# Kernel tuning notes

Measured on AMD Instinct MI355X. Metric: run time of the kernel, lower is better.

## Reference

```python
import jax, jax.numpy as jnp
import numpy as np

BATCH, IN, OUT, P = 8192, 1024, 1024, 8

def setup_inputs() -> dict:
    key = jax.random.key(0)
    k1, k2, k3 = jax.random.split(key, 3)
    x = jax.random.normal(k1, (BATCH, IN), dtype=jnp.float32)
    # per-(output,input) basis coefficients, init ~ randn*0.1 as in torch module
    coefficients = jax.random.normal(k2, (OUT, IN, P), dtype=jnp.float32) * 0.1
    weights = jax.random.normal(k3, (OUT, IN), dtype=jnp.float32)
    return {"x": x, "coefficients": coefficients, "weights": weights}

def reference(x, coefficients, weights):
    # out[b,o] = sum_i x[b,i] * (sum_p coef[o,i,p]) * weights[o,i]
    # == x @ (coef_sum * weights)^T  -- single fused GEMM
    w_eff = coefficients.sum(axis=-1) * weights  # [O, I]
    return jnp.einsum('bi,oi->bo', x, w_eff)
```

## Files before the change

kernel.cpp:

```cpp
#include <hip/hip_runtime.h>
#include <hip/hip_bf16.h>
#include <stdint.h>

#define BATCH 8192
#define IN    1024
#define OUTD  1024
#define PBASIS 8

typedef __attribute__((ext_vector_type(8))) short bf16x8;
typedef __attribute__((ext_vector_type(4))) float floatx4;

__device__ __forceinline__ unsigned short f2bf(float f) {
    union { float f; unsigned u; } v; v.f = f;
    unsigned u = v.u;
    u += 0x7fffu + ((u >> 16) & 1u);
    return (unsigned short)(u >> 16);
}

__global__ void prep_kernel(const float* __restrict__ x,
                            const float* __restrict__ coef,
                            const float* __restrict__ w,
                            unsigned short* __restrict__ xb,
                            unsigned short* __restrict__ weff) {
    int b = blockIdx.x;
    int tid = threadIdx.x;
    if (b < 4096) {
        int idx = b * 256 + tid;
        const float4* p = (const float4*)(x + (size_t)idx * 8);
        float4 a = p[0], c = p[1];
        uint4 o;
        o.x = (unsigned)f2bf(a.x) | ((unsigned)f2bf(a.y) << 16);
        o.y = (unsigned)f2bf(a.z) | ((unsigned)f2bf(a.w) << 16);
        o.z = (unsigned)f2bf(c.x) | ((unsigned)f2bf(c.y) << 16);
        o.w = (unsigned)f2bf(c.z) | ((unsigned)f2bf(c.w) << 16);
        ((uint4*)xb)[idx] = o;
    } else {
        int idx = (b - 4096) * 256 + tid;
        size_t e0 = (size_t)idx * 2;
        const float4* c4 = (const float4*)(coef + e0 * PBASIS);
        float4 a = c4[0], bb = c4[1], c = c4[2], d = c4[3];
        float s0 = (a.x + a.y + a.z + a.w) + (bb.x + bb.y + bb.z + bb.w);
        float s1 = (c.x + c.y + c.z + c.w) + (d.x + d.y + d.z + d.w);
        float2 ww = ((const float2*)w)[idx];
        unsigned b0 = f2bf(s0 * ww.x);
        unsigned b1 = f2bf(s1 * ww.y);
        ((unsigned*)weff)[idx] = b0 | (b1 << 16);
    }
}

__global__ __launch_bounds__(256, 2) void gemm_bt(
        const unsigned short* __restrict__ A,
        const unsigned short* __restrict__ B,
        float* __restrict__ C) {
    constexpr int K = IN, BK = 64;
    constexpr int ES = 132;
    __shared__ __align__(16) char smem[32768];
    unsigned short* As = (unsigned short*)smem;
    unsigned short* Bs = As + 128 * BK;
    float* ebuf = (float*)smem;

    const int tid  = threadIdx.x;
    const int bm   = blockIdx.x, bn = blockIdx.y;
    const int lane = tid & 63;
    const int wave = tid >> 6;
    const int wm   = wave & 1, wn = wave >> 1;
    const int t    = lane & 15;
    const int q    = lane >> 4;
    const int r8   = t & 7;

    int G0 = tid,       r0 = G0 >> 3, c0 = G0 & 7, s0i = r0 * 8 + (c0 ^ (r0 & 7));
    int G1 = 256 + tid, r1 = G1 >> 3, c1 = G1 & 7, s1i = r1 * 8 + (c1 ^ (r1 & 7));
    int G2 = 512 + tid, r2 = G2 >> 3, c2 = G2 & 7, s2i = r2 * 8 + (c2 ^ (r2 & 7));
    int G3 = 768 + tid, r3 = G3 >> 3, c3 = G3 & 7, s3i = r3 * 8 + (c3 ^ (r3 & 7));

    const unsigned short* gA0 = A + (size_t)(bm * 128 + r0) * K + c0 * 8;
    const unsigned short* gA1 = A + (size_t)(bm * 128 + r1) * K + c1 * 8;
    const unsigned short* gA2 = A + (size_t)(bm * 128 + r2) * K + c2 * 8;
    const unsigned short* gA3 = A + (size_t)(bm * 128 + r3) * K + c3 * 8;
    const unsigned short* gB0 = B + (size_t)(bn * 128 + r0) * K + c0 * 8;
    const unsigned short* gB1 = B + (size_t)(bn * 128 + r1) * K + c1 * 8;
    const unsigned short* gB2 = B + (size_t)(bn * 128 + r2) * K + c2 * 8;
    const unsigned short* gB3 = B + (size_t)(bn * 128 + r3) * K + c3 * 8;

    unsigned short* lA0 = As + s0i * 8;  unsigned short* lB0 = Bs + s0i * 8;
    unsigned short* lA1 = As + s1i * 8;  unsigned short* lB1 = Bs + s1i * 8;
    unsigned short* lA2 = As + s2i * 8;  unsigned short* lB2 = Bs + s2i * 8;
    unsigned short* lA3 = As + s3i * 8;  unsigned short* lB3 = Bs + s3i * 8;

    const unsigned short* aB0 = As + (wm * 64 + t) * BK + ((0 + q) ^ r8) * 8;
    const unsigned short* aB1 = As + (wm * 64 + t) * BK + ((4 + q) ^ r8) * 8;
    const unsigned short* bB0 = Bs + (wn * 64 + t) * BK + ((0 + q) ^ r8) * 8;
    const unsigned short* bB1 = Bs + (wn * 64 + t) * BK + ((4 + q) ^ r8) * 8;

    floatx4 acc[4][4];
#pragma unroll
    for (int i = 0; i < 4; ++i)
#pragma unroll
        for (int j = 0; j < 4; ++j)
            acc[i][j] = (floatx4){0.f, 0.f, 0.f, 0.f};

#define COMPUTE()                                                   \
    {                                                               \
        bf16x8 af0, af1, af2, af3, ag0, ag1, ag2, ag3;              \
        bf16x8 bf0, bf1, bf2, bf3, bg0, bg1, bg2, bg3;              \
        af0 = *(const bf16x8*)(aB0 + 0 * 1024);                     \
        af1 = *(const bf16x8*)(aB0 + 1 * 1024);                     \
        af2 = *(const bf16x8*)(aB0 + 2 * 1024);                     \
        af3 = *(const bf16x8*)(aB0 + 3 * 1024);                     \
        ag0 = *(const bf16x8*)(aB1 + 0 * 1024);                     \
        ag1 = *(const bf16x8*)(aB1 + 1 * 1024);                     \
        ag2 = *(const bf16x8*)(aB1 + 2 * 1024);                     \
        ag3 = *(const bf16x8*)(aB1 + 3 * 1024);                     \
        bf0 = *(const bf16x8*)(bB0 + 0 * 1024);                     \
        bf1 = *(const bf16x8*)(bB0 + 1 * 1024);                     \
        bf2 = *(const bf16x8*)(bB0 + 2 * 1024);                     \
        bf3 = *(const bf16x8*)(bB0 + 3 * 1024);                     \
        bg0 = *(const bf16x8*)(bB1 + 0 * 1024);                     \
        bg1 = *(const bf16x8*)(bB1 + 1 * 1024);                     \
        bg2 = *(const bf16x8*)(bB1 + 2 * 1024);                     \
        bg3 = *(const bf16x8*)(bB1 + 3 * 1024);                     \
        bf16x8 afv[4] = {af0, af1, af2, af3};                       \
        bf16x8 agv[4] = {ag0, ag1, ag2, ag3};                       \
        bf16x8 bfv[4] = {bf0, bf1, bf2, bf3};                       \
        bf16x8 bgv[4] = {bg0, bg1, bg2, bg3};                       \
        _Pragma("unroll")                                           \
        for (int i = 0; i < 4; ++i)                                 \
            _Pragma("unroll")                                       \
            for (int j = 0; j < 4; ++j) {                           \
                acc[i][j] = __builtin_amdgcn_mfma_f32_16x16x32_bf16(\
                    afv[i], bfv[j], acc[i][j], 0, 0, 0);            \
                acc[i][j] = __builtin_amdgcn_mfma_f32_16x16x32_bf16(\
                    agv[i], bgv[j], acc[i][j], 0, 0, 0);            \
            }                                                       \
    }

    uint4 ca0, ca1, ca2, ca3, cb0, cb1, cb2, cb3;
    uint4 pa0, pa1, pa2, pa3, pb0, pb1, pb2, pb3;

    ca0 = *(const uint4*)gA0; ca1 = *(const uint4*)gA1;
    ca2 = *(const uint4*)gA2; ca3 = *(const uint4*)gA3;
    cb0 = *(const uint4*)gB0; cb1 = *(const uint4*)gB1;
    cb2 = *(const uint4*)gB2; cb3 = *(const uint4*)gB3;

    for (int it = 0; it < K / (2 * BK); ++it) {
        const int k1 = ((2 * it + 1) * BK);
        const int k2 = ((2 * it + 2) * BK) & (K - 1);
        *(uint4*)lA0 = ca0; *(uint4*)lA1 = ca1; *(uint4*)lA2 = ca2; *(uint4*)lA3 = ca3;
        *(uint4*)lB0 = cb0; *(uint4*)lB1 = cb1; *(uint4*)lB2 = cb2; *(uint4*)lB3 = cb3;
        __syncthreads();
        pa0 = *(const uint4*)(gA0 + k1); pa1 = *(const uint4*)(gA1 + k1);
        pa2 = *(const uint4*)(gA2 + k1); pa3 = *(const uint4*)(gA3 + k1);
        pb0 = *(const uint4*)(gB0 + k1); pb1 = *(const uint4*)(gB1 + k1);
        pb2 = *(const uint4*)(gB2 + k1); pb3 = *(const uint4*)(gB3 + k1);
        COMPUTE();
        __syncthreads();
        *(uint4*)lA0 = pa0; *(uint4*)lA1 = pa1; *(uint4*)lA2 = pa2; *(uint4*)lA3 = pa3;
        *(uint4*)lB0 = pb0; *(uint4*)lB1 = pb1; *(uint4*)lB2 = pb2; *(uint4*)lB3 = pb3;
        __syncthreads();
        ca0 = *(const uint4*)(gA0 + k2); ca1 = *(const uint4*)(gA1 + k2);
        ca2 = *(const uint4*)(gA2 + k2); ca3 = *(const uint4*)(gA3 + k2);
        cb0 = *(const uint4*)(gB0 + k2); cb1 = *(const uint4*)(gB1 + k2);
        cb2 = *(const uint4*)(gB2 + k2); cb3 = *(const uint4*)(gB3 + k2);
        COMPUTE();
        __syncthreads();
    }
#undef COMPUTE

#pragma unroll
    for (int p = 0; p < 4; ++p) {
        if (p) __syncthreads();
        if (wm == (p >> 1)) {
            int dt = p & 1;
#pragma unroll
            for (int half = 0; half < 2; ++half) {
                int tm = dt * 2 + half;
#pragma unroll
                for (int tn = 0; tn < 4; ++tn) {
                    int col = wn * 64 + tn * 16 + t;
#pragma unroll
                    for (int r = 0; r < 4; ++r) {
                        int brow = half * 16 + q * 4 + r;
                        ebuf[brow * ES + col] = acc[tm][tn][r];
                    }
                }
            }
        }
        __syncthreads();
#pragma unroll
        for (int rr = 0; rr < 4; ++rr) {
            int brow = rr * 8 + (tid >> 5);
            int col4 = tid & 31;
            float4 v = *(const float4*)(ebuf + brow * ES + col4 * 4);
            size_t grow = (size_t)(bm * 128 + p * 32 + brow);
            *(float4*)(C + grow * OUTD + bn * 128 + col4 * 4) = v;
        }
    }
}

extern "C" void kernel_launch(void* const* d_in, const int* in_sizes, int n_in,
                              void* d_out, int out_size, void* d_ws, size_t ws_size,
                              hipStream_t stream) {
    const float* x    = (const float*)d_in[0];
    const float* coef = (const float*)d_in[1];
    const float* w    = (const float*)d_in[2];
    float* out = (float*)d_out;

    unsigned short* xb   = (unsigned short*)d_ws;
    unsigned short* weff = (unsigned short*)((char*)d_ws + (size_t)BATCH * IN * 2);

    prep_kernel<<<6144, 256, 0, stream>>>(x, coef, w, xb, weff);
    gemm_bt<<<dim3(BATCH / 128, OUTD / 128), 256, 0, stream>>>(xb, weff, out);
}
```

Before: 125.3 us.

## Load GEMM tiles directly into LDS with global_load_lds, dropping register prefetch

Replaces the register-staged global loads and LDS stores with direct global-to-LDS loads (global_load_lds, 16 bytes). The XOR swizzle moves from the LDS destination to the global source column. This removes the VGPR staging and the ds_write instructions. It also drops the software prefetch that overlapped the next tile's global loads with the MFMA compute, so each iteration now waits on its load before computing.

New measurement: 126.6 us. About the same (+1.0%).

```diff
diff --git a/kernel.cpp b/kernel.cpp
--- a/kernel.cpp
+++ b/kernel.cpp
@@ -48,6 +48,13 @@
     }
 }
 
+__device__ __forceinline__ void gload_lds16(const void* g, void* l) {
+    __builtin_amdgcn_global_load_lds(
+        (const __attribute__((address_space(1))) unsigned int*)g,
+        (__attribute__((address_space(3))) unsigned int*)l,
+        16, 0, 0);
+}
+
 __global__ __launch_bounds__(256, 2) void gemm_bt(
         const unsigned short* __restrict__ A,
         const unsigned short* __restrict__ B,
@@ -68,24 +75,24 @@
     const int q    = lane >> 4;
     const int r8   = t & 7;
 
-    int G0 = tid,       r0 = G0 >> 3, c0 = G0 & 7, s0i = r0 * 8 + (c0 ^ (r0 & 7));
-    int G1 = 256 + tid, r1 = G1 >> 3, c1 = G1 & 7, s1i = r1 * 8 + (c1 ^ (r1 & 7));
-    int G2 = 512 + tid, r2 = G2 >> 3, c2 = G2 & 7, s2i = r2 * 8 + (c2 ^ (r2 & 7));
-    int G3 = 768 + tid, r3 = G3 >> 3, c3 = G3 & 7, s3i = r3 * 8 + (c3 ^ (r3 & 7));
-
-    const unsigned short* gA0 = A + (size_t)(bm * 128 + r0) * K + c0 * 8;
-    const unsigned short* gA1 = A + (size_t)(bm * 128 + r1) * K + c1 * 8;
-    const unsigned short* gA2 = A + (size_t)(bm * 128 + r2) * K + c2 * 8;
-    const unsigned short* gA3 = A + (size_t)(bm * 128 + r3) * K + c3 * 8;
-    const unsigned short* gB0 = B + (size_t)(bn * 128 + r0) * K + c0 * 8;
-    const unsigned short* gB1 = B + (size_t)(bn * 128 + r1) * K + c1 * 8;
-    const unsigned short* gB2 = B + (size_t)(bn * 128 + r2) * K + c2 * 8;
-    const unsigned short* gB3 = B + (size_t)(bn * 128 + r3) * K + c3 * 8;
-
-    unsigned short* lA0 = As + s0i * 8;  unsigned short* lB0 = Bs + s0i * 8;
-    unsigned short* lA1 = As + s1i * 8;  unsigned short* lB1 = Bs + s1i * 8;
-    unsigned short* lA2 = As + s2i * 8;  unsigned short* lB2 = Bs + s2i * 8;
-    unsigned short* lA3 = As + s3i * 8;  unsigned short* lB3 = Bs + s3i * 8;
+    int g0 = tid,       r0 = g0 >> 3, cs0 = (g0 & 7) ^ (r0 & 7);
+    int g1 = 256 + tid, r1 = g1 >> 3, cs1 = (g1 & 7) ^ (r1 & 7);
+    int g2 = 512 + tid, r2 = g2 >> 3, cs2 = (g2 & 7) ^ (r2 & 7);
+    int g3 = 768 + tid, r3 = g3 >> 3, cs3 = (g3 & 7) ^ (r3 & 7);
+
+    const unsigned short* gA0 = A + (size_t)(bm * 128 + r0) * K + cs0 * 8;
+    const unsigned short* gA1 = A + (size_t)(bm * 128 + r1) * K + cs1 * 8;
+    const unsigned short* gA2 = A + (size_t)(bm * 128 + r2) * K + cs2 * 8;
+    const unsigned short* gA3 = A + (size_t)(bm * 128 + r3) * K + cs3 * 8;
+    const unsigned short* gB0 = B + (size_t)(bn * 128 + r0) * K + cs0 * 8;
+    const unsigned short* gB1 = B + (size_t)(bn * 128 + r1) * K + cs1 * 8;
+    const unsigned short* gB2 = B + (size_t)(bn * 128 + r2) * K + cs2 * 8;
+    const unsigned short* gB3 = B + (size_t)(bn * 128 + r3) * K + cs3 * 8;
+
+    unsigned short* dA0 = As + g0 * 8;  unsigned short* dB0 = Bs + g0 * 8;
+    unsigned short* dA1 = As + g1 * 8;  unsigned short* dB1 = Bs + g1 * 8;
+    unsigned short* dA2 = As + g2 * 8;  unsigned short* dB2 = Bs + g2 * 8;
+    unsigned short* dA3 = As + g3 * 8;  unsigned short* dB3 = Bs + g3 * 8;
 
     const unsigned short* aB0 = As + (wm * 64 + t) * BK + ((0 + q) ^ r8) * 8;
     const unsigned short* aB1 = As + (wm * 64 + t) * BK + ((4 + q) ^ r8) * 8;
@@ -134,33 +141,17 @@
             }                                                       \
     }
 
-    uint4 ca0, ca1, ca2, ca3, cb0, cb1, cb2, cb3;
-    uint4 pa0, pa1, pa2, pa3, pb0, pb1, pb2, pb3;
-
-    ca0 = *(const uint4*)gA0; ca1 = *(const uint4*)gA1;
-    ca2 = *(const uint4*)gA2; ca3 = *(const uint4*)gA3;
-    cb0 = *(const uint4*)gB0; cb1 = *(const uint4*)gB1;
-    cb2 = *(const uint4*)gB2; cb3 = *(const uint4*)gB3;
-
-    for (int it = 0; it < K / (2 * BK); ++it) {
-        const int k1 = ((2 * it + 1) * BK);
-        const int k2 = ((2 * it + 2) * BK) & (K - 1);
-        *(uint4*)lA0 = ca0; *(uint4*)lA1 = ca1; *(uint4*)lA2 = ca2; *(uint4*)lA3 = ca3;
-        *(uint4*)lB0 = cb0; *(uint4*)lB1 = cb1; *(uint4*)lB2 = cb2; *(uint4*)lB3 = cb3;
+    for (int kt = 0; kt < K / BK; ++kt) {
+        const int k0 = kt * BK;
+        gload_lds16(gA0 + k0, dA0);
+        gload_lds16(gA1 + k0, dA1);
+        gload_lds16(gA2 + k0, dA2);
+        gload_lds16(gA3 + k0, dA3);
+        gload_lds16(gB0 + k0, dB0);
+        gload_lds16(gB1 + k0, dB1);
+        gload_lds16(gB2 + k0, dB2);
+        gload_lds16(gB3 + k0, dB3);
         __syncthreads();
-        pa0 = *(const uint4*)(gA0 + k1); pa1 = *(const uint4*)(gA1 + k1);
-        pa2 = *(const uint4*)(gA2 + k1); pa3 = *(const uint4*)(gA3 + k1);
-        pb0 = *(const uint4*)(gB0 + k1); pb1 = *(const uint4*)(gB1 + k1);
-        pb2 = *(const uint4*)(gB2 + k1); pb3 = *(const uint4*)(gB3 + k1);
-        COMPUTE();
-        __syncthreads();
-        *(uint4*)lA0 = pa0; *(uint4*)lA1 = pa1; *(uint4*)lA2 = pa2; *(uint4*)lA3 = pa3;
-        *(uint4*)lB0 = pb0; *(uint4*)lB1 = pb1; *(uint4*)lB2 = pb2; *(uint4*)lB3 = pb3;
-        __syncthreads();
-        ca0 = *(const uint4*)(gA0 + k2); ca1 = *(const uint4*)(gA1 + k2);
-        ca2 = *(const uint4*)(gA2 + k2); ca3 = *(const uint4*)(gA3 + k2);
-        cb0 = *(const uint4*)(gB0 + k2); cb1 = *(const uint4*)(gB1 + k2);
-        cb2 = *(const uint4*)(gB2 + k2); cb3 = *(const uint4*)(gB3 + k2);
         COMPUTE();
         __syncthreads();
     }
```
